# Performance work log

Hardware: AMD Instinct MI355X
Metric: run time of the kernel (lower is better)

Reference implementation:

```python
import jax, jax.numpy as jnp
import numpy as np

LORA_R = 16
SCALE = 16.0 / np.sqrt(16.0)  # rsLoRA: alpha / sqrt(r) = 4.0
NUM_EXPERTS = 4
TOP_K = 2
IN_F = 4096
OUT_F = 4096


def setup_inputs() -> dict:
    key = jax.random.key(0)
    k_x, k_a, k_b, k_r = jax.random.split(key, 4)
    x = jax.random.normal(k_x, (2, 2048, IN_F), dtype=jnp.float32)
    # Stacked expert weights: A [E, R, in_f], B [E, out_f, R]
    # (B is zero-initialized in the original; use small randn so the output is non-trivial)
    A = jax.random.normal(k_a, (NUM_EXPERTS, LORA_R, IN_F), dtype=jnp.float32) * (1.0 / np.sqrt(IN_F))
    B = jax.random.normal(k_b, (NUM_EXPERTS, OUT_F, LORA_R), dtype=jnp.float32) * 0.02
    Wr = jax.random.normal(k_r, (NUM_EXPERTS, IN_F), dtype=jnp.float32) * 0.02  # router weight
    return {"x": x, "A": A, "B": B, "Wr": Wr}


def reference(x, A, B, Wr):
    orig_shape = x.shape
    flat = x.reshape(-1, orig_shape[-1])              # [T, F]
    logits = flat @ Wr.T                              # [T, E]
    topk_vals, topk_idx = jax.lax.top_k(logits, TOP_K)  # [T, K]
    T = flat.shape[0]
    neg_inf = jnp.finfo(logits.dtype).min
    sparse = jnp.full_like(logits, neg_inf)
    rows = jnp.arange(T)[:, None]
    sparse = sparse.at[rows, topk_idx].set(topk_vals)
    gates = jax.nn.softmax(sparse, axis=-1)           # [T, E]
    mid = jnp.einsum('tf,erf->ter', flat, A)          # [T, E, R]
    all_deltas = jnp.einsum('ter,eor->teo', mid, B) * SCALE  # [T, E, O]
    delta = jnp.sum(gates[:, :, None] * all_deltas, axis=1)  # [T, O]
    return delta.reshape(*orig_shape[:-1], -1)
```

## Files before the change

### kernel.cpp

```cpp
#include <hip/hip_runtime.h>

#define T_TOKENS 4096
#define F_IN 4096
#define O_OUT 4096
#define SCALE_F 4.0f

typedef __attribute__((ext_vector_type(8))) short bf16x8;
typedef __attribute__((ext_vector_type(4))) float f32x4;
typedef __attribute__((ext_vector_type(4))) int i32x4;

#define WBM_E 0
#define WRB_E 262144
#define BB_E  327680

__device__ __forceinline__ unsigned short f2bf(float f) {
    unsigned u = __float_as_uint(f);
    return (unsigned short)((u + 0x7fffu + ((u >> 16) & 1u)) >> 16);
}
__device__ __forceinline__ float bf2f(unsigned short h) {
    return __uint_as_float(((unsigned)h) << 16);
}
__device__ __forceinline__ int cvt_pk(float a, float b) {
    int r;
    asm("v_cvt_pk_bf16_f32 %0, %1, %2" : "=v"(r) : "v"(a), "v"(b));
    return r;
}

__global__ __launch_bounds__(256) void kprep(const float* __restrict__ A,
                                             const float* __restrict__ Wr,
                                             const float* __restrict__ B,
                                             unsigned short* __restrict__ ws) {
    const int f = blockIdx.x * 256 + threadIdx.x;
    if (f < 32768) {
        const int kb8 = f >> 6, c = f & 63;
        const float* src = A + (size_t)c * F_IN + kb8 * 8;
        float4 a = *(const float4*)src, b = *(const float4*)(src + 4);
        i32x4 v;
        v[0] = cvt_pk(a.x, a.y); v[1] = cvt_pk(a.z, a.w);
        v[2] = cvt_pk(b.x, b.y); v[3] = cvt_pk(b.z, b.w);
        *(i32x4*)(ws + WBM_E + (size_t)f * 8) = v;
    } else if (f < 40960) {
        const int j = f - 32768;
        const int kb8 = j >> 4, cc = j & 15;
        bf16x8 v = {0,0,0,0,0,0,0,0};
        if (cc < 8) {
            const float* src = Wr + (size_t)(cc & 3) * F_IN + kb8 * 8;
            float4 a = *(const float4*)src, b = *(const float4*)(src + 4);
            float ff[8] = {a.x, a.y, a.z, a.w, b.x, b.y, b.z, b.w};
            if (cc < 4) {
#pragma unroll
                for (int q = 0; q < 8; ++q) v[q] = (short)f2bf(ff[q]);
            } else {
#pragma unroll
                for (int q = 0; q < 8; ++q) {
                    unsigned short h = f2bf(ff[q]);
                    v[q] = (short)f2bf(ff[q] - bf2f(h));
                }
            }
        }
        *(bf16x8*)(ws + WRB_E + (size_t)j * 8) = v;
    } else if (f < 73728) {
        const int j = f - 40960;
        const int kb8 = j >> 12, o = j & 4095;
        const float* src = B + ((size_t)(kb8 >> 1) * O_OUT + o) * 16 + (kb8 & 1) * 8;
        float4 a = *(const float4*)src, b = *(const float4*)(src + 4);
        i32x4 v;
        v[0] = cvt_pk(a.x, a.y); v[1] = cvt_pk(a.z, a.w);
        v[2] = cvt_pk(b.x, b.y); v[3] = cvt_pk(b.z, b.w);
        *(i32x4*)(ws + BB_E + (size_t)j * 8) = v;
    }
}

__global__ __launch_bounds__(512) void kfused(const float* __restrict__ x,
                                              const unsigned short* __restrict__ wpack,
                                              float* __restrict__ out) {
    const int tid = threadIdx.x;
    const int w = tid >> 6, l = tid & 63, lm = l & 15, lk = l >> 4;
    const int tb = (int)blockIdx.x * 16;
    const int kbase = w * 512;

    const bf16x8* wbm8 = (const bf16x8*)(wpack + WBM_E);
    const bf16x8* wrb8 = (const bf16x8*)(wpack + WRB_E);
    const bf16x8* bb8  = (const bf16x8*)(wpack + BB_E);

    f32x4 am0 = {0.f,0.f,0.f,0.f}, am1 = am0, am2 = am0, am3 = am0;
    f32x4 ar0 = am0, ar1 = am0;
    const float* xrow = x + (size_t)(tb + lm) * F_IN;

#pragma unroll 4
    for (int s = 0; s < 16; ++s) {
        const int kc = kbase + s * 32 + lk * 8;
        float4 xa = *(const float4*)(xrow + kc);
        float4 xb = *(const float4*)(xrow + kc + 4);
        float f[8] = {xa.x, xa.y, xa.z, xa.w, xb.x, xb.y, xb.z, xb.w};
        i32x4 hi_i, lo_i;
#pragma unroll
        for (int p = 0; p < 4; ++p) {
            float a = f[2*p], b = f[2*p+1];
            int pk = cvt_pk(a, b);
            float la = a - __uint_as_float(((unsigned)pk) << 16);
            float lb = b - __uint_as_float((unsigned)pk & 0xffff0000u);
            hi_i[p] = pk;
            lo_i[p] = cvt_pk(la, lb);
        }
        bf16x8 xhi = __builtin_bit_cast(bf16x8, hi_i);
        bf16x8 xlo = __builtin_bit_cast(bf16x8, lo_i);

        const int kb8 = kc >> 3;
        bf16x8 w0 = wbm8[kb8 * 64 +  0 + lm];
        bf16x8 w1 = wbm8[kb8 * 64 + 16 + lm];
        bf16x8 w2 = wbm8[kb8 * 64 + 32 + lm];
        bf16x8 w3 = wbm8[kb8 * 64 + 48 + lm];
        bf16x8 wr = wrb8[kb8 * 16 + lm];
        am0 = __builtin_amdgcn_mfma_f32_16x16x32_bf16(xhi, w0, am0, 0, 0, 0);
        am1 = __builtin_amdgcn_mfma_f32_16x16x32_bf16(xhi, w1, am1, 0, 0, 0);
        am2 = __builtin_amdgcn_mfma_f32_16x16x32_bf16(xhi, w2, am2, 0, 0, 0);
        am3 = __builtin_amdgcn_mfma_f32_16x16x32_bf16(xhi, w3, am3, 0, 0, 0);
        ar0 = __builtin_amdgcn_mfma_f32_16x16x32_bf16(xhi, wr, ar0, 0, 0, 0);
        ar1 = __builtin_amdgcn_mfma_f32_16x16x32_bf16(xlo, wr, ar1, 0, 0, 0);
    }

    __shared__ float red[8][6][64][4];
    __shared__ float mids[16][68];
    __shared__ float lgp[2][16][16];
    __shared__ float gl[16][4];
    __shared__ __align__(16) unsigned short mfr[8 * 16 * 8];

    *(f32x4*)&red[w][0][l][0] = am0;
    *(f32x4*)&red[w][1][l][0] = am1;
    *(f32x4*)&red[w][2][l][0] = am2;
    *(f32x4*)&red[w][3][l][0] = am3;
    *(f32x4*)&red[w][4][l][0] = ar0;
    *(f32x4*)&red[w][5][l][0] = ar1;
    __syncthreads();

#pragma unroll
    for (int it = 0; it < 3; ++it) {
        int j = tid + it * 512;
        int tile = j >> 8, rem = j & 255, rl = rem >> 2, q = rem & 3;
        float s = 0.f;
#pragma unroll
        for (int ww = 0; ww < 8; ++ww) s += red[ww][tile][rl][q];
        int token = ((rl >> 4) << 2) + q, c = rl & 15;
        if (tile < 4) mids[token][tile * 16 + c] = s;
        else          lgp[tile - 4][token][c] = s;
    }
    __syncthreads();

    if (tid < 16) {
        float lg[4];
#pragma unroll
        for (int e = 0; e < 4; ++e)
            lg[e] = lgp[0][tid][e] + lgp[0][tid][4 + e]
                  + lgp[1][tid][e] + lgp[1][tid][4 + e];
        int i1 = 0; float m1 = lg[0];
#pragma unroll
        for (int e = 1; e < 4; ++e)
            if (lg[e] > m1) { m1 = lg[e]; i1 = e; }
        int i2 = -1; float m2 = 0.f;
#pragma unroll
        for (int e = 0; e < 4; ++e)
            if (e != i1 && (i2 < 0 || lg[e] > m2)) { m2 = lg[e]; i2 = e; }
        float ex = __expf(m2 - m1);
        float inv = 1.f / (1.f + ex);
#pragma unroll
        for (int e = 0; e < 4; ++e) gl[tid][e] = 0.f;
        gl[tid][i1] = inv * SCALE_F;
        gl[tid][i2] = ex * inv * SCALE_F;
    }
    __syncthreads();

    {
        int t = tid & 15, kp = tid >> 4;
        int k0 = kp * 2;
        float g = gl[t][k0 >> 4];
        int pk = cvt_pk(mids[t][k0] * g, mids[t][k0 + 1] * g);
        *(int*)&mfr[((k0 >> 3) * 16 + t) * 8 + (k0 & 7)] = pk;
    }
    __syncthreads();

    const int ob = w * 512;
    const bf16x8* mf8 = (const bf16x8*)mfr;
    bf16x8 ma0 = mf8[(0 + lk) * 16 + lm];
    bf16x8 ma1 = mf8[(4 + lk) * 16 + lm];

#pragma unroll 4
    for (int n = 0; n < 32; ++n) {
        const int oc = ob + n * 16;
        bf16x8 b0 = bb8[(size_t)lk * 4096 + oc + lm];
        bf16x8 b1 = bb8[(size_t)(4 + lk) * 4096 + oc + lm];
        f32x4 acc = {0.f,0.f,0.f,0.f};
        acc = __builtin_amdgcn_mfma_f32_16x16x32_bf16(ma0, b0, acc, 0, 0, 0);
        acc = __builtin_amdgcn_mfma_f32_16x16x32_bf16(ma1, b1, acc, 0, 0, 0);
#pragma unroll
        for (int q = 0; q < 4; ++q)
            out[(size_t)(tb + lk * 4 + q) * O_OUT + oc + lm] = acc[q];
    }
}

extern "C" void kernel_launch(void* const* d_in, const int* in_sizes, int n_in,
                              void* d_out, int out_size, void* d_ws, size_t ws_size,
                              hipStream_t stream) {
    const float* x  = (const float*)d_in[0];
    const float* A  = (const float*)d_in[1];
    const float* B  = (const float*)d_in[2];
    const float* Wr = (const float*)d_in[3];
    float* out = (float*)d_out;
    unsigned short* wsu = (unsigned short*)d_ws;

    kprep<<<288, 256, 0, stream>>>(A, Wr, B, wsu);
    kfused<<<256, 512, 0, stream>>>(x, wsu, out);
}
```

Before: 37.98 us.

## Split fused LoRA kernel into split-K mid kernel and tiled output kernel

Replaces the single fused kernel with two kernels. The first splits the K dimension in half across twice as many blocks and writes partial mids and router logits to a workspace buffer. The second sums the partials, computes the top-2 gates, and produces 64-token by 256-column output tiles across 1024 blocks. The aim is more parallelism on the memory-bound x read and the output write, at the cost of an extra launch and a round trip of the partials through global memory.

```diff
diff --git a/kernel.cpp b/kernel.cpp
--- a/kernel.cpp
+++ b/kernel.cpp
@@ -12,6 +12,7 @@
 #define WBM_E 0
 #define WRB_E 262144
 #define BB_E  327680
+#define PART_F 294912
 
 __device__ __forceinline__ unsigned short f2bf(float f) {
     unsigned u = __float_as_uint(f);
@@ -71,24 +72,24 @@
     }
 }
 
-__global__ __launch_bounds__(512) void kfused(const float* __restrict__ x,
+__global__ __launch_bounds__(512) void k1_mid(const float* __restrict__ x,
                                               const unsigned short* __restrict__ wpack,
-                                              float* __restrict__ out) {
+                                              float* __restrict__ partial) {
     const int tid = threadIdx.x;
     const int w = tid >> 6, l = tid & 63, lm = l & 15, lk = l >> 4;
-    const int tb = (int)blockIdx.x * 16;
-    const int kbase = w * 512;
+    const int tg = (int)blockIdx.x >> 1, kh = (int)blockIdx.x & 1;
+    const int tb = tg * 16;
+    const int kbase = kh * 2048 + w * 256;
 
     const bf16x8* wbm8 = (const bf16x8*)(wpack + WBM_E);
     const bf16x8* wrb8 = (const bf16x8*)(wpack + WRB_E);
-    const bf16x8* bb8  = (const bf16x8*)(wpack + BB_E);
 
     f32x4 am0 = {0.f,0.f,0.f,0.f}, am1 = am0, am2 = am0, am3 = am0;
     f32x4 ar0 = am0, ar1 = am0;
     const float* xrow = x + (size_t)(tb + lm) * F_IN;
 
-#pragma unroll 4
-    for (int s = 0; s < 16; ++s) {
+#pragma unroll
+    for (int s = 0; s < 8; ++s) {
         const int kc = kbase + s * 32 + lk * 8;
         float4 xa = *(const float4*)(xrow + kc);
         float4 xb = *(const float4*)(xrow + kc + 4);
@@ -121,11 +122,6 @@
     }
 
     __shared__ float red[8][6][64][4];
-    __shared__ float mids[16][68];
-    __shared__ float lgp[2][16][16];
-    __shared__ float gl[16][4];
-    __shared__ __align__(16) unsigned short mfr[8 * 16 * 8];
-
     *(f32x4*)&red[w][0][l][0] = am0;
     *(f32x4*)&red[w][1][l][0] = am1;
     *(f32x4*)&red[w][2][l][0] = am2;
@@ -142,17 +138,50 @@
 #pragma unroll
         for (int ww = 0; ww < 8; ++ww) s += red[ww][tile][rl][q];
         int token = ((rl >> 4) << 2) + q, c = rl & 15;
-        if (tile < 4) mids[token][tile * 16 + c] = s;
-        else          lgp[tile - 4][token][c] = s;
-    }
-    __syncthreads();
-
-    if (tid < 16) {
+        int col;
+        if (tile < 4)      col = tile * 16 + c;
+        else if (c < 8)    col = (tile == 4 ? 64 : 72) + c;
+        else               col = -1;
+        if (col >= 0)
+            partial[(size_t)kh * T_TOKENS * 80 + (size_t)(tb + token) * 80 + col] = s;
+    }
+}
+
+__global__ __launch_bounds__(256) void k2_out(const float* __restrict__ partial,
+                                              const unsigned short* __restrict__ wpack,
+                                              float* __restrict__ out) {
+    const int tid = threadIdx.x;
+    const int tb = ((int)blockIdx.x >> 4) * 64;
+    const int ob = ((int)blockIdx.x & 15) * 256;
+
+    __shared__ float mids[64][64];
+    __shared__ float lgq[64][4][4];
+    __shared__ float gl[64][4];
+    __shared__ __align__(16) unsigned short mfr[8][64][8];
+
+    const f32x4* p4 = (const f32x4*)partial;
+    const int KHS = T_TOKENS * 20;
+
+#pragma unroll
+    for (int i = 0; i < 4; ++i) {
+        int idx = tid + i * 256;
+        int t = idx >> 4, c4 = idx & 15;
+        f32x4 v = p4[(size_t)(tb + t) * 20 + c4] + p4[(size_t)KHS + (tb + t) * 20 + c4];
+        *(f32x4*)&mids[t][c4 * 4] = v;
+    }
+    {
+        int t = tid >> 2, g = tid & 3;
+        f32x4 v = p4[(size_t)(tb + t) * 20 + 16 + g] + p4[(size_t)KHS + (tb + t) * 20 + 16 + g];
+        *(f32x4*)&lgq[t][g][0] = v;
+    }
+    __syncthreads();
+
+    if (tid < 64) {
+        const int t = tid;
         float lg[4];
 #pragma unroll
         for (int e = 0; e < 4; ++e)
-            lg[e] = lgp[0][tid][e] + lgp[0][tid][4 + e]
-                  + lgp[1][tid][e] + lgp[1][tid][4 + e];
+            lg[e] = lgq[t][0][e] + lgq[t][1][e] + lgq[t][2][e] + lgq[t][3][e];
         int i1 = 0; float m1 = lg[0];
 #pragma unroll
         for (int e = 1; e < 4; ++e)
@@ -164,37 +193,38 @@
         float ex = __expf(m2 - m1);
         float inv = 1.f / (1.f + ex);
 #pragma unroll
-        for (int e = 0; e < 4; ++e) gl[tid][e] = 0.f;
-        gl[tid][i1] = inv * SCALE_F;
-        gl[tid][i2] = ex * inv * SCALE_F;
-    }
-    __syncthreads();
-
-    {
-        int t = tid & 15, kp = tid >> 4;
-        int k0 = kp * 2;
+        for (int e = 0; e < 4; ++e) gl[t][e] = 0.f;
+        gl[t][i1] = inv * SCALE_F;
+        gl[t][i2] = ex * inv * SCALE_F;
+    }
+    __syncthreads();
+
+#pragma unroll
+    for (int i = 0; i < 8; ++i) {
+        int j = tid + i * 256;
+        int t = j >> 5, kp = j & 31, k0 = kp * 2;
         float g = gl[t][k0 >> 4];
         int pk = cvt_pk(mids[t][k0] * g, mids[t][k0 + 1] * g);
-        *(int*)&mfr[((k0 >> 3) * 16 + t) * 8 + (k0 & 7)] = pk;
-    }
-    __syncthreads();
-
-    const int ob = w * 512;
-    const bf16x8* mf8 = (const bf16x8*)mfr;
-    bf16x8 ma0 = mf8[(0 + lk) * 16 + lm];
-    bf16x8 ma1 = mf8[(4 + lk) * 16 + lm];
+        *(int*)&mfr[k0 >> 3][t][k0 & 7] = pk;
+    }
+    __syncthreads();
+
+    const int w = tid >> 6, l = tid & 63, lm = l & 15, lk = l >> 4;
+    const bf16x8* bb8 = (const bf16x8*)(wpack + BB_E);
+    const bf16x8 p0 = *(const bf16x8*)&mfr[lk][w * 16 + lm][0];
+    const bf16x8 p1 = *(const bf16x8*)&mfr[4 + lk][w * 16 + lm][0];
 
 #pragma unroll 4
-    for (int n = 0; n < 32; ++n) {
+    for (int n = 0; n < 16; ++n) {
         const int oc = ob + n * 16;
         bf16x8 b0 = bb8[(size_t)lk * 4096 + oc + lm];
         bf16x8 b1 = bb8[(size_t)(4 + lk) * 4096 + oc + lm];
         f32x4 acc = {0.f,0.f,0.f,0.f};
-        acc = __builtin_amdgcn_mfma_f32_16x16x32_bf16(ma0, b0, acc, 0, 0, 0);
-        acc = __builtin_amdgcn_mfma_f32_16x16x32_bf16(ma1, b1, acc, 0, 0, 0);
+        acc = __builtin_amdgcn_mfma_f32_16x16x32_bf16(p0, b0, acc, 0, 0, 0);
+        acc = __builtin_amdgcn_mfma_f32_16x16x32_bf16(p1, b1, acc, 0, 0, 0);
 #pragma unroll
         for (int q = 0; q < 4; ++q)
-            out[(size_t)(tb + lk * 4 + q) * O_OUT + oc + lm] = acc[q];
+            out[(size_t)(tb + w * 16 + lk * 4 + q) * O_OUT + oc + lm] = acc[q];
     }
 }
 
@@ -207,7 +237,9 @@
     const float* Wr = (const float*)d_in[3];
     float* out = (float*)d_out;
     unsigned short* wsu = (unsigned short*)d_ws;
+    float* partial = (float*)d_ws + PART_F;
 
     kprep<<<288, 256, 0, stream>>>(A, Wr, B, wsu);
-    kfused<<<256, 512, 0, stream>>>(x, wsu, out);
-}
+    k1_mid<<<512, 512, 0, stream>>>(x, wsu, partial);
+    k2_out<<<1024, 256, 0, stream>>>(partial, wsu, out);
+}
```

Measured after the change: 42.15 us. 11.0% more time.

## Prefetch all x loads up front and store output as float4 via swapped MFMA operands

Applied to the files above, without the earlier changes.

The phase-1 loop is fully unrolled, and all 32 float4 loads of x for each lane are issued before any MFMA work. This exposes more memory-level parallelism and hides global load latency. In phase 2 the MFMA operands are swapped so each lane holds four consecutive output columns of one token, letting the output be written with a single float4 store instead of four scalar stores. The cost is much higher register pressure from holding 128 floats of x per thread, which could cut occupancy or cause spills.

```diff
diff --git a/kernel.cpp b/kernel.cpp
--- a/kernel.cpp
+++ b/kernel.cpp
@@ -71,6 +71,37 @@
     }
 }
 
+__device__ __forceinline__ void ph1_step(float4 xa, float4 xb, int kb8, int lm,
+                                         const bf16x8* __restrict__ wbm8,
+                                         const bf16x8* __restrict__ wrb8,
+                                         f32x4& am0, f32x4& am1, f32x4& am2,
+                                         f32x4& am3, f32x4& ar0, f32x4& ar1) {
+    float f[8] = {xa.x, xa.y, xa.z, xa.w, xb.x, xb.y, xb.z, xb.w};
+    i32x4 hi_i, lo_i;
+#pragma unroll
+    for (int p = 0; p < 4; ++p) {
+        float a = f[2*p], b = f[2*p+1];
+        int pk = cvt_pk(a, b);
+        float la = a - __uint_as_float(((unsigned)pk) << 16);
+        float lb = b - __uint_as_float((unsigned)pk & 0xffff0000u);
+        hi_i[p] = pk;
+        lo_i[p] = cvt_pk(la, lb);
+    }
+    bf16x8 xhi = __builtin_bit_cast(bf16x8, hi_i);
+    bf16x8 xlo = __builtin_bit_cast(bf16x8, lo_i);
+    bf16x8 w0 = wbm8[kb8 * 64 +  0 + lm];
+    bf16x8 w1 = wbm8[kb8 * 64 + 16 + lm];
+    bf16x8 w2 = wbm8[kb8 * 64 + 32 + lm];
+    bf16x8 w3 = wbm8[kb8 * 64 + 48 + lm];
+    bf16x8 wr = wrb8[kb8 * 16 + lm];
+    am0 = __builtin_amdgcn_mfma_f32_16x16x32_bf16(xhi, w0, am0, 0, 0, 0);
+    am1 = __builtin_amdgcn_mfma_f32_16x16x32_bf16(xhi, w1, am1, 0, 0, 0);
+    am2 = __builtin_amdgcn_mfma_f32_16x16x32_bf16(xhi, w2, am2, 0, 0, 0);
+    am3 = __builtin_amdgcn_mfma_f32_16x16x32_bf16(xhi, w3, am3, 0, 0, 0);
+    ar0 = __builtin_amdgcn_mfma_f32_16x16x32_bf16(xhi, wr, ar0, 0, 0, 0);
+    ar1 = __builtin_amdgcn_mfma_f32_16x16x32_bf16(xlo, wr, ar1, 0, 0, 0);
+}
+
 __global__ __launch_bounds__(512) void kfused(const float* __restrict__ x,
                                               const unsigned short* __restrict__ wpack,
                                               float* __restrict__ out) {
@@ -85,46 +116,34 @@
 
     f32x4 am0 = {0.f,0.f,0.f,0.f}, am1 = am0, am2 = am0, am3 = am0;
     f32x4 ar0 = am0, ar1 = am0;
-    const float* xrow = x + (size_t)(tb + lm) * F_IN;
-
-#pragma unroll 4
-    for (int s = 0; s < 16; ++s) {
-        const int kc = kbase + s * 32 + lk * 8;
-        float4 xa = *(const float4*)(xrow + kc);
-        float4 xb = *(const float4*)(xrow + kc + 4);
-        float f[8] = {xa.x, xa.y, xa.z, xa.w, xb.x, xb.y, xb.z, xb.w};
-        i32x4 hi_i, lo_i;
-#pragma unroll
-        for (int p = 0; p < 4; ++p) {
-            float a = f[2*p], b = f[2*p+1];
-            int pk = cvt_pk(a, b);
-            float la = a - __uint_as_float(((unsigned)pk) << 16);
-            float lb = b - __uint_as_float((unsigned)pk & 0xffff0000u);
-            hi_i[p] = pk;
-            lo_i[p] = cvt_pk(la, lb);
-        }
-        bf16x8 xhi = __builtin_bit_cast(bf16x8, hi_i);
-        bf16x8 xlo = __builtin_bit_cast(bf16x8, lo_i);
-
-        const int kb8 = kc >> 3;
-        bf16x8 w0 = wbm8[kb8 * 64 +  0 + lm];
-        bf16x8 w1 = wbm8[kb8 * 64 + 16 + lm];
-        bf16x8 w2 = wbm8[kb8 * 64 + 32 + lm];
-        bf16x8 w3 = wbm8[kb8 * 64 + 48 + lm];
-        bf16x8 wr = wrb8[kb8 * 16 + lm];
-        am0 = __builtin_amdgcn_mfma_f32_16x16x32_bf16(xhi, w0, am0, 0, 0, 0);
-        am1 = __builtin_amdgcn_mfma_f32_16x16x32_bf16(xhi, w1, am1, 0, 0, 0);
-        am2 = __builtin_amdgcn_mfma_f32_16x16x32_bf16(xhi, w2, am2, 0, 0, 0);
-        am3 = __builtin_amdgcn_mfma_f32_16x16x32_bf16(xhi, w3, am3, 0, 0, 0);
-        ar0 = __builtin_amdgcn_mfma_f32_16x16x32_bf16(xhi, wr, ar0, 0, 0, 0);
-        ar1 = __builtin_amdgcn_mfma_f32_16x16x32_bf16(xlo, wr, ar1, 0, 0, 0);
-    }
+    const float* xrow = x + (size_t)(tb + lm) * F_IN + kbase + lk * 8;
+    const int kb80 = (kbase >> 3) + lk;
+
+    float4 xA[16], xB[16];
+#pragma unroll
+    for (int j = 0; j < 8; ++j) {
+        xA[2*j]   = *(const float4*)(xrow + j * 32);
+        xA[2*j+1] = *(const float4*)(xrow + j * 32 + 4);
+    }
+#pragma unroll
+    for (int j = 0; j < 8; ++j) {
+        xB[2*j]   = *(const float4*)(xrow + 256 + j * 32);
+        xB[2*j+1] = *(const float4*)(xrow + 256 + j * 32 + 4);
+    }
+#pragma unroll
+    for (int j = 0; j < 8; ++j)
+        ph1_step(xA[2*j], xA[2*j+1], kb80 + j * 4, lm, wbm8, wrb8,
+                 am0, am1, am2, am3, ar0, ar1);
+#pragma unroll
+    for (int j = 0; j < 8; ++j)
+        ph1_step(xB[2*j], xB[2*j+1], kb80 + 32 + j * 4, lm, wbm8, wrb8,
+                 am0, am1, am2, am3, ar0, ar1);
 
     __shared__ float red[8][6][64][4];
     __shared__ float mids[16][68];
     __shared__ float lgp[2][16][16];
     __shared__ float gl[16][4];
-    __shared__ __align__(16) unsigned short mfr[8 * 16 * 8];
+    __shared__ __align__(16) unsigned short mfr[8][16][8];
 
     *(f32x4*)&red[w][0][l][0] = am0;
     *(f32x4*)&red[w][1][l][0] = am1;
@@ -175,14 +194,13 @@
         int k0 = kp * 2;
         float g = gl[t][k0 >> 4];
         int pk = cvt_pk(mids[t][k0] * g, mids[t][k0 + 1] * g);
-        *(int*)&mfr[((k0 >> 3) * 16 + t) * 8 + (k0 & 7)] = pk;
+        *(int*)&mfr[k0 >> 3][t][k0 & 7] = pk;
     }
     __syncthreads();
 
     const int ob = w * 512;
-    const bf16x8* mf8 = (const bf16x8*)mfr;
-    bf16x8 ma0 = mf8[(0 + lk) * 16 + lm];
-    bf16x8 ma1 = mf8[(4 + lk) * 16 + lm];
+    const bf16x8 p0 = *(const bf16x8*)&mfr[lk][lm][0];
+    const bf16x8 p1 = *(const bf16x8*)&mfr[4 + lk][lm][0];
 
 #pragma unroll 4
     for (int n = 0; n < 32; ++n) {
@@ -190,11 +208,10 @@
         bf16x8 b0 = bb8[(size_t)lk * 4096 + oc + lm];
         bf16x8 b1 = bb8[(size_t)(4 + lk) * 4096 + oc + lm];
         f32x4 acc = {0.f,0.f,0.f,0.f};
-        acc = __builtin_amdgcn_mfma_f32_16x16x32_bf16(ma0, b0, acc, 0, 0, 0);
-        acc = __builtin_amdgcn_mfma_f32_16x16x32_bf16(ma1, b1, acc, 0, 0, 0);
-#pragma unroll
-        for (int q = 0; q < 4; ++q)
-            out[(size_t)(tb + lk * 4 + q) * O_OUT + oc + lm] = acc[q];
+        acc = __builtin_amdgcn_mfma_f32_16x16x32_bf16(b0, p0, acc, 0, 0, 0);
+        acc = __builtin_amdgcn_mfma_f32_16x16x32_bf16(b1, p1, acc, 0, 0, 0);
+        float4 r4 = make_float4(acc[0], acc[1], acc[2], acc[3]);
+        *(float4*)&out[(size_t)(tb + lm) * O_OUT + oc + lk * 4] = r4;
     }
 }
 
```

Measured after the change: 39.25 us. 3.4% more time.
